# Kernel optimization log

Measured on AMD Instinct MI355X. Metric: run time of the kernel, lower is better.

Reference implementation:

```python
import jax, jax.numpy as jnp
import numpy as np

P_FACTOR = 3.0
EPS = 1e-12  # torch F.normalize eps


def _l2_normalize(x):
    # matches torch.nn.functional.normalize(x, dim=-1): x / max(||x||, eps)
    n = jnp.linalg.norm(x, axis=-1, keepdims=True)
    return x / jnp.maximum(n, EPS)


def setup_inputs() -> dict:
    key = jax.random.key(0)
    k1, k2, k3 = jax.random.split(key, 3)
    N, D, H, C = 8192, 16384, 256, 28
    return {
        "features": jax.random.normal(k1, (N, H), dtype=jnp.float32),
        "ex_features": jax.random.normal(k2, (D, H), dtype=jnp.float32),
        "ex_class_reps": jax.random.normal(k3, (D, C), dtype=jnp.float32),
    }


def reference(features, ex_features, ex_class_reps):
    # cosine similarity: [N, D]
    s = _l2_normalize(features) @ _l2_normalize(ex_features).T
    # power-law activation: |s|^p * sign(s)
    a = jnp.power(jnp.abs(s), P_FACTOR) * jnp.sign(s)
    intensity = a.sum(axis=1)               # [N]
    echo = a @ ex_class_reps                # [N, C]
    return (echo, intensity)
```

## Files before the change

### kernel.cpp

```cpp
#include <hip/hip_runtime.h>
#include <stdint.h>


typedef unsigned short u16;
typedef __bf16 bf16x8 __attribute__((ext_vector_type(8)));
typedef float f32x4 __attribute__((ext_vector_type(4)));
typedef unsigned short u16x4 __attribute__((ext_vector_type(4)));

#define NQ 8192
#define ND 16384
#define NH 256
#define NC 28
#define DCHUNK 2048
#define NDT 32
#define NSLOT 8

__device__ __forceinline__ u16 f2bf(float f) {
  unsigned u = __builtin_bit_cast(unsigned, f);
  u += 0x7fffu + ((u >> 16) & 1u);
  return (u16)(u >> 16);
}

__device__ __forceinline__ unsigned cvtpk(float lo, float hi) {
  unsigned r;
  asm("v_cvt_pk_bf16_f32 %0, %1, %2" : "=v"(r) : "v"(lo), "v"(hi));
  return r;
}

__device__ __forceinline__ void swap2(unsigned& x, unsigned& y) {
  asm("v_permlane32_swap_b32 %0, %1" : "+v"(x), "+v"(y));
  asm("v_permlane16_swap_b32 %0, %1" : "+v"(x), "+v"(y));
}

__device__ __forceinline__ void gload16(const void* g, void* l) {
  __builtin_amdgcn_global_load_lds(
      (__attribute__((address_space(1))) void*)g,
      (__attribute__((address_space(3))) void*)l, 16, 0, 0);
}

__global__ __launch_bounds__(256) void prep_kernel(
    const float* __restrict__ feat, const float* __restrict__ exf,
    const float* __restrict__ V, u16* __restrict__ qn, u16* __restrict__ kn,
    u16* __restrict__ Vt) {
  if (blockIdx.x < 6144) {
    const int wid = threadIdx.x >> 6, lane = threadIdx.x & 63;
    const int row = blockIdx.x * 4 + wid;
    const float* in = (row < NQ) ? feat + (size_t)row * NH
                                 : exf + (size_t)(row - NQ) * NH;
    u16* out = (row < NQ) ? qn + (size_t)row * NH : kn + (size_t)(row - NQ) * NH;
    float4 v = ((const float4*)in)[lane];
    float ss = v.x * v.x + v.y * v.y + v.z * v.z + v.w * v.w;
#pragma unroll
    for (int m = 1; m <= 32; m <<= 1) ss += __shfl_xor(ss, m, 64);
    const float sc = 1.0f / fmaxf(sqrtf(ss), 1e-12f);
    u16x4 o;
    o.x = f2bf(v.x * sc); o.y = f2bf(v.y * sc);
    o.z = f2bf(v.z * sc); o.w = f2bf(v.w * sc);
    *(u16x4*)(out + lane * 4) = o;
  } else {
    const int d = (blockIdx.x - 6144) * 256 + threadIdx.x;
#pragma unroll
    for (int c = 0; c < NC; ++c) Vt[(size_t)c * ND + d] = f2bf(V[(size_t)d * NC + c]);
    Vt[(size_t)28 * ND + d] = 0x3F80;
    Vt[(size_t)29 * ND + d] = 0;
    Vt[(size_t)30 * ND + d] = 0;
    Vt[(size_t)31 * ND + d] = 0;
  }
}

__global__ __launch_bounds__(256, 2) void fused_kernel(
    const u16* __restrict__ Qn, const u16* __restrict__ Kn,
    const u16* __restrict__ Vt, float* __restrict__ ep) {
  __shared__ alignas(16) char smem[65536];
  const int tid = threadIdx.x;
  const int wid = tid >> 6;
  const int lane = tid & 63;
  const int l16 = lane & 15;
  const int lg = lane >> 4;
  const int wr = wid >> 1;
  const int wd = wid & 1;
  const int dch = blockIdx.x & 7;
  const int ntile = blockIdx.x >> 3;
  const int rowbase = ntile * 128 + wr * 64;

  bf16x8 qA[4][8];
#pragma unroll
  for (int mb = 0; mb < 4; ++mb)
#pragma unroll
    for (int ks = 0; ks < 8; ++ks)
      qA[mb][ks] = *(const bf16x8*)(Qn + (size_t)(rowbase + mb * 16 + l16) * NH +
                                    ks * 32 + lg * 8);

  f32x4 eacc[4][2];
#pragma unroll
  for (int mb = 0; mb < 4; ++mb) {
    eacc[mb][0] = f32x4{0.f, 0.f, 0.f, 0.f};
    eacc[mb][1] = f32x4{0.f, 0.f, 0.f, 0.f};
  }
  f32x4 sacc[4][2];

  const u16* kc = Kn + (size_t)dch * DCHUNK * NH;
  const int srow = (tid >> 6) * 16 + ((tid >> 2) & 15);
  const u16* kb = kc + (size_t)srow * NH + ((tid & 3) ^ ((tid >> 3) & 3)) * 8;

  auto stage = [&](int buf, const u16* src0) {
#pragma unroll
    for (int r = 0; r < 8; ++r)
      gload16(src0 + r * 32,
              smem + buf * 32768 + r * 4096 + wid * 1024);
  };

  const int rsw = (l16 >> 1) & 3;

  auto compute = [&](int buf) {
    const char* kbuf = smem + buf * 32768;
#pragma unroll
    for (int k2 = 0; k2 < 8; ++k2) {
      bf16x8 B[2];
#pragma unroll
      for (int nb = 0; nb < 2; ++nb)
        B[nb] = *(const bf16x8*)(kbuf + k2 * 4096 + (wd * 32 + nb * 16 + l16) * 64 +
                                 ((lg ^ rsw) << 4));
      __builtin_amdgcn_s_setprio(1);
#pragma unroll
      for (int mb = 0; mb < 4; ++mb)
#pragma unroll
        for (int nb = 0; nb < 2; ++nb)
          sacc[mb][nb] = __builtin_amdgcn_mfma_f32_16x16x32_bf16(
              B[nb], qA[mb][k2], sacc[mb][nb], 0, 0, 0);
      __builtin_amdgcn_s_setprio(0);
    }
  };

  stage(0, kb);
  __syncthreads();

  for (int t = 0; t < NDT; ++t) {
    const int cur = t & 1;
    const int dbase = dch * DCHUNK + t * 64 + wd * 32;

#pragma unroll
    for (int mb = 0; mb < 4; ++mb) {
      sacc[mb][0] = f32x4{0.f, 0.f, 0.f, 0.f};
      sacc[mb][1] = f32x4{0.f, 0.f, 0.f, 0.f};
    }

    if (t < NDT - 1) stage(cur ^ 1, kb + (size_t)(t + 1) * 64 * NH);

    bf16x8 vB[2];
#pragma unroll
    for (int cn = 0; cn < 2; ++cn)
      vB[cn] = *(const bf16x8*)(Vt + (size_t)(cn * 16 + l16) * ND + dbase + lg * 8);

    compute(cur);

#pragma unroll
    for (int mb = 0; mb < 4; ++mb) {
      f32x4 sx = sacc[mb][0];
      f32x4 sy = sacc[mb][1];
      f32x4 cx = sx * sx * sx;
      f32x4 cy = sy * sy * sy;
      unsigned x0 = cvtpk(cx[0], cx[1]);
      unsigned x1 = cvtpk(cx[2], cx[3]);
      unsigned y0 = cvtpk(cy[0], cy[1]);
      unsigned y1 = cvtpk(cy[2], cy[3]);
      swap2(x0, y0);
      swap2(x1, y1);
      const int4 ai = {(int)x0, (int)x1, (int)y0, (int)y1};
      const bf16x8 aA = __builtin_bit_cast(bf16x8, ai);
#pragma unroll
      for (int cn = 0; cn < 2; ++cn)
        eacc[mb][cn] = __builtin_amdgcn_mfma_f32_16x16x32_bf16(
            aA, vB[cn], eacc[mb][cn], 0, 0, 0);
    }

    __syncthreads();
  }

  float* eml = (float*)smem;
  if (wd == 1) {
    float* dst = eml + (wr * 64 + lane) * 36;
#pragma unroll
    for (int mb = 0; mb < 4; ++mb)
#pragma unroll
      for (int cn = 0; cn < 2; ++cn)
        *(f32x4*)(dst + (mb * 2 + cn) * 4) = eacc[mb][cn];
  }
  __syncthreads();
  if (wd == 0) {
    const float* src = eml + (wr * 64 + lane) * 36;
#pragma unroll
    for (int mb = 0; mb < 4; ++mb)
#pragma unroll
      for (int cn = 0; cn < 2; ++cn) {
        const f32x4 m = eacc[mb][cn] + *(const f32x4*)(src + (mb * 2 + cn) * 4);
#pragma unroll
        for (int r = 0; r < 4; ++r) {
          const int row = rowbase + mb * 16 + lg * 4 + r;
          ep[((size_t)dch * NQ + row) * 32 + cn * 16 + l16] = m[r];
        }
      }
  }
}

__global__ __launch_bounds__(256) void reduce_kernel(const float* __restrict__ ep,
                                                     float* __restrict__ out) {
  const int g = blockIdx.x * 256 + threadIdx.x;
  const int q = g >> 5, c = g & 31;
  if (c < NC) {
    float s = 0.f;
#pragma unroll
    for (int k = 0; k < NSLOT; ++k) s += ep[((size_t)k * NQ + q) * 32 + c];
    out[(size_t)q * NC + c] = s;
  } else if (c == NC) {
    float s = 0.f;
#pragma unroll
    for (int k = 0; k < NSLOT; ++k) s += ep[((size_t)k * NQ + q) * 32 + NC];
    out[(size_t)NQ * NC + q] = s;
  }
}

extern "C" void kernel_launch(void* const* d_in, const int* in_sizes, int n_in,
                              void* d_out, int out_size, void* d_ws, size_t ws_size,
                              hipStream_t stream) {
  const float* feat = (const float*)d_in[0];
  const float* exf  = (const float*)d_in[1];
  const float* exc  = (const float*)d_in[2];
  float* out = (float*)d_out;
  char* ws = (char*)d_ws;
  u16* qn = (u16*)ws;
  u16* kn = (u16*)(ws + 4194304);
  u16* vt = (u16*)(ws + 12582912);
  float* ep = (float*)(ws + 13631488);

  prep_kernel<<<dim3(6208), dim3(256), 0, stream>>>(feat, exf, exc, qn, kn, vt);
  fused_kernel<<<dim3(512), dim3(256), 0, stream>>>(qn, kn, vt, ep);
  reduce_kernel<<<dim3(NQ * 32 / 256), dim3(256), 0, stream>>>(ep, out);
}
```

Before: 82.03 us.

## Switch fused similarity and echo matmuls to 32x32x16 MFMA tiles

Replaces the 16x16x32 bf16 MFMA tiling with 32x32x16 instructions for both the similarity GEMM and the cubed-activation times V GEMM. The register layout of Q fragments, the accumulators, and the permlane shuffle that turns S accumulators into A operands are reworked, with only a 32-lane swap needed now. The aim is fewer MFMA issues and LDS reads per unit of work, since the larger instruction has higher per-issue throughput and better operand reuse. The risk is higher register pressure from 16-wide accumulators and a changed LDS read pattern that may cause bank conflicts.

```diff
diff --git a/kernel.cpp b/kernel.cpp
--- a/kernel.cpp
+++ b/kernel.cpp
@@ -5,6 +5,7 @@
 typedef unsigned short u16;
 typedef __bf16 bf16x8 __attribute__((ext_vector_type(8)));
 typedef float f32x4 __attribute__((ext_vector_type(4)));
+typedef float f32x16 __attribute__((ext_vector_type(16)));
 typedef unsigned short u16x4 __attribute__((ext_vector_type(4)));
 
 #define NQ 8192
@@ -27,9 +28,8 @@
   return r;
 }
 
-__device__ __forceinline__ void swap2(unsigned& x, unsigned& y) {
+__device__ __forceinline__ void swap32(unsigned& x, unsigned& y) {
   asm("v_permlane32_swap_b32 %0, %1" : "+v"(x), "+v"(y));
-  asm("v_permlane16_swap_b32 %0, %1" : "+v"(x), "+v"(y));
 }
 
 __device__ __forceinline__ void gload16(const void* g, void* l) {
@@ -75,29 +75,28 @@
   const int tid = threadIdx.x;
   const int wid = tid >> 6;
   const int lane = tid & 63;
-  const int l16 = lane & 15;
-  const int lg = lane >> 4;
+  const int lane31 = lane & 31;
+  const int lhalf = lane >> 5;
   const int wr = wid >> 1;
   const int wd = wid & 1;
   const int dch = blockIdx.x & 7;
   const int ntile = blockIdx.x >> 3;
   const int rowbase = ntile * 128 + wr * 64;
 
-  bf16x8 qA[4][8];
-#pragma unroll
-  for (int mb = 0; mb < 4; ++mb)
-#pragma unroll
-    for (int ks = 0; ks < 8; ++ks)
-      qA[mb][ks] = *(const bf16x8*)(Qn + (size_t)(rowbase + mb * 16 + l16) * NH +
-                                    ks * 32 + lg * 8);
-
-  f32x4 eacc[4][2];
-#pragma unroll
-  for (int mb = 0; mb < 4; ++mb) {
-    eacc[mb][0] = f32x4{0.f, 0.f, 0.f, 0.f};
-    eacc[mb][1] = f32x4{0.f, 0.f, 0.f, 0.f};
-  }
-  f32x4 sacc[4][2];
+  bf16x8 qB[2][16];
+#pragma unroll
+  for (int qh = 0; qh < 2; ++qh)
+#pragma unroll
+    for (int ks = 0; ks < 16; ++ks)
+      qB[qh][ks] = *(const bf16x8*)(Qn + (size_t)(rowbase + qh * 32 + lane31) * NH +
+                                    ks * 16 + lhalf * 8);
+
+  f32x16 eacc32[2];
+  f32x16 pacc[2];
+#pragma unroll
+  for (int qh = 0; qh < 2; ++qh)
+#pragma unroll
+    for (int r = 0; r < 16; ++r) eacc32[qh][r] = 0.f;
 
   const u16* kc = Kn + (size_t)dch * DCHUNK * NH;
   const int srow = (tid >> 6) * 16 + ((tid >> 2) & 15);
@@ -110,25 +109,24 @@
               smem + buf * 32768 + r * 4096 + wid * 1024);
   };
 
-  const int rsw = (l16 >> 1) & 3;
+  const int rsw32 = (lane31 >> 1) & 3;
 
   auto compute = [&](int buf) {
     const char* kbuf = smem + buf * 32768;
 #pragma unroll
-    for (int k2 = 0; k2 < 8; ++k2) {
-      bf16x8 B[2];
-#pragma unroll
-      for (int nb = 0; nb < 2; ++nb)
-        B[nb] = *(const bf16x8*)(kbuf + k2 * 4096 + (wd * 32 + nb * 16 + l16) * 64 +
-                                 ((lg ^ rsw) << 4));
-      __builtin_amdgcn_s_setprio(1);
-#pragma unroll
-      for (int mb = 0; mb < 4; ++mb)
-#pragma unroll
-        for (int nb = 0; nb < 2; ++nb)
-          sacc[mb][nb] = __builtin_amdgcn_mfma_f32_16x16x32_bf16(
-              B[nb], qA[mb][k2], sacc[mb][nb], 0, 0, 0);
-      __builtin_amdgcn_s_setprio(0);
+    for (int kp = 0; kp < 8; ++kp) {
+#pragma unroll
+      for (int h = 0; h < 2; ++h) {
+        const bf16x8 A = *(const bf16x8*)(
+            kbuf + kp * 4096 + (wd * 32 + lane31) * 64 +
+            (((h * 2 + lhalf) ^ rsw32) << 4));
+        __builtin_amdgcn_s_setprio(1);
+        pacc[0] = __builtin_amdgcn_mfma_f32_32x32x16_bf16(
+            A, qB[0][kp * 2 + h], pacc[0], 0, 0, 0);
+        pacc[1] = __builtin_amdgcn_mfma_f32_32x32x16_bf16(
+            A, qB[1][kp * 2 + h], pacc[1], 0, 0, 0);
+        __builtin_amdgcn_s_setprio(0);
+      }
     }
   };
 
@@ -140,38 +138,41 @@
     const int dbase = dch * DCHUNK + t * 64 + wd * 32;
 
 #pragma unroll
-    for (int mb = 0; mb < 4; ++mb) {
-      sacc[mb][0] = f32x4{0.f, 0.f, 0.f, 0.f};
-      sacc[mb][1] = f32x4{0.f, 0.f, 0.f, 0.f};
-    }
+    for (int qh = 0; qh < 2; ++qh)
+#pragma unroll
+      for (int r = 0; r < 16; ++r) pacc[qh][r] = 0.f;
 
     if (t < NDT - 1) stage(cur ^ 1, kb + (size_t)(t + 1) * 64 * NH);
 
     bf16x8 vB[2];
 #pragma unroll
-    for (int cn = 0; cn < 2; ++cn)
-      vB[cn] = *(const bf16x8*)(Vt + (size_t)(cn * 16 + l16) * ND + dbase + lg * 8);
+    for (int w = 0; w < 2; ++w)
+      vB[w] = *(const bf16x8*)(Vt + (size_t)lane31 * ND + dbase + w * 16 +
+                               lhalf * 8);
 
     compute(cur);
 
 #pragma unroll
-    for (int mb = 0; mb < 4; ++mb) {
-      f32x4 sx = sacc[mb][0];
-      f32x4 sy = sacc[mb][1];
-      f32x4 cx = sx * sx * sx;
-      f32x4 cy = sy * sy * sy;
-      unsigned x0 = cvtpk(cx[0], cx[1]);
-      unsigned x1 = cvtpk(cx[2], cx[3]);
-      unsigned y0 = cvtpk(cy[0], cy[1]);
-      unsigned y1 = cvtpk(cy[2], cy[3]);
-      swap2(x0, y0);
-      swap2(x1, y1);
-      const int4 ai = {(int)x0, (int)x1, (int)y0, (int)y1};
-      const bf16x8 aA = __builtin_bit_cast(bf16x8, ai);
-#pragma unroll
-      for (int cn = 0; cn < 2; ++cn)
-        eacc[mb][cn] = __builtin_amdgcn_mfma_f32_16x16x32_bf16(
-            aA, vB[cn], eacc[mb][cn], 0, 0, 0);
+    for (int qh = 0; qh < 2; ++qh) {
+      float c[16];
+#pragma unroll
+      for (int r = 0; r < 16; ++r) {
+        const float s = pacc[qh][r];
+        c[r] = s * s * s;
+      }
+#pragma unroll
+      for (int w = 0; w < 2; ++w) {
+        unsigned x0 = cvtpk(c[8 * w + 0], c[8 * w + 1]);
+        unsigned x1 = cvtpk(c[8 * w + 2], c[8 * w + 3]);
+        unsigned y0 = cvtpk(c[8 * w + 4], c[8 * w + 5]);
+        unsigned y1 = cvtpk(c[8 * w + 6], c[8 * w + 7]);
+        swap32(x0, y0);
+        swap32(x1, y1);
+        const int4 ai = {(int)x0, (int)x1, (int)y0, (int)y1};
+        const bf16x8 aA = __builtin_bit_cast(bf16x8, ai);
+        eacc32[qh] = __builtin_amdgcn_mfma_f32_32x32x16_bf16(
+            aA, vB[w], eacc32[qh], 0, 0, 0);
+      }
     }
 
     __syncthreads();
@@ -179,26 +180,25 @@
 
   float* eml = (float*)smem;
   if (wd == 1) {
-    float* dst = eml + (wr * 64 + lane) * 36;
-#pragma unroll
-    for (int mb = 0; mb < 4; ++mb)
-#pragma unroll
-      for (int cn = 0; cn < 2; ++cn)
-        *(f32x4*)(dst + (mb * 2 + cn) * 4) = eacc[mb][cn];
+    float* dst = eml + (wr * 64 + lane) * 32;
+#pragma unroll
+    for (int qh = 0; qh < 2; ++qh)
+#pragma unroll
+      for (int r = 0; r < 4; ++r)
+        *(f32x4*)(dst + qh * 16 + r * 4) =
+            f32x4{eacc32[qh][r * 4], eacc32[qh][r * 4 + 1],
+                  eacc32[qh][r * 4 + 2], eacc32[qh][r * 4 + 3]};
   }
   __syncthreads();
   if (wd == 0) {
-    const float* src = eml + (wr * 64 + lane) * 36;
-#pragma unroll
-    for (int mb = 0; mb < 4; ++mb)
-#pragma unroll
-      for (int cn = 0; cn < 2; ++cn) {
-        const f32x4 m = eacc[mb][cn] + *(const f32x4*)(src + (mb * 2 + cn) * 4);
-#pragma unroll
-        for (int r = 0; r < 4; ++r) {
-          const int row = rowbase + mb * 16 + lg * 4 + r;
-          ep[((size_t)dch * NQ + row) * 32 + cn * 16 + l16] = m[r];
-        }
+    const float* src = eml + (wr * 64 + lane) * 32;
+#pragma unroll
+    for (int qh = 0; qh < 2; ++qh)
+#pragma unroll
+      for (int r = 0; r < 16; ++r) {
+        const float m = eacc32[qh][r] + src[qh * 16 + r];
+        const int row = rowbase + qh * 32 + (r & 3) + 8 * (r >> 2) + 4 * lhalf;
+        ep[((size_t)dch * NQ + row) * 32 + lane31] = m;
       }
   }
 }
```

New measurement: 90.34 us. 1.1x slower.
